# Optimization experiments

Measured on AMD Instinct MI355X. Metric: run time of the kernel, lower is better.

The kernel has to match this reference:

```python
import jax, jax.numpy as jnp
import numpy as np

NUM_ITEMS = 50000
IN_FEATS = 64
H_FEATS = 64
NUM_EDGES = 800000


def setup_inputs() -> dict:
    key = jax.random.key(0)
    ks = jax.random.split(key, 12)
    s_in = 1.0 / np.sqrt(IN_FEATS)
    s_h = 1.0 / np.sqrt(H_FEATS)
    return {
        "embed": jax.random.normal(ks[0], (NUM_ITEMS, IN_FEATS), jnp.float32),
        "W1_self": jax.random.normal(ks[1], (IN_FEATS, H_FEATS), jnp.float32) * s_in,
        "W1_neigh": jax.random.normal(ks[2], (IN_FEATS, H_FEATS), jnp.float32) * s_in,
        "b1": jax.random.normal(ks[3], (H_FEATS,), jnp.float32) * s_in,
        "W2_self": jax.random.normal(ks[4], (H_FEATS, H_FEATS), jnp.float32) * s_h,
        "W2_neigh": jax.random.normal(ks[5], (H_FEATS, H_FEATS), jnp.float32) * s_h,
        "b2": jax.random.normal(ks[6], (H_FEATS,), jnp.float32) * s_h,
        "W_fc": jax.random.normal(ks[7], (H_FEATS, IN_FEATS), jnp.float32) * s_h,
        "b_fc": jax.random.normal(ks[8], (IN_FEATS,), jnp.float32) * s_h,
        "item_ids": jnp.arange(NUM_ITEMS, dtype=jnp.int64),
        "src": jax.random.randint(ks[9], (NUM_EDGES,), 0, NUM_ITEMS, jnp.int64),
        "dst": jax.random.randint(ks[10], (NUM_EDGES,), 0, NUM_ITEMS, jnp.int64),
    }


def _sage_mean(h, src, dst, W_self, W_neigh, b, num_nodes):
    # gather src features along edges, mean-reduce into dst nodes
    agg = jax.ops.segment_sum(h[src], dst, num_segments=num_nodes)  # [N, d]
    deg = jax.ops.segment_sum(jnp.ones_like(dst, dtype=h.dtype), dst,
                              num_segments=num_nodes)
    h_neigh = agg / jnp.clip(deg, 1.0, None)[:, None]  # zero for isolated nodes
    return h @ W_self + h_neigh @ W_neigh + b


def reference(embed, W1_self, W1_neigh, b1, W2_self, W2_neigh, b2,
              W_fc, b_fc, item_ids, src, dst):
    n = embed.shape[0]
    x = embed[item_ids]                                   # embedding lookup [N, in]
    h = _sage_mean(x, src, dst, W1_self, W1_neigh, b1, n)  # SAGEConv 1
    h = jax.nn.relu(h)
    h = _sage_mean(h, src, dst, W2_self, W2_neigh, b2, n)  # SAGEConv 2
    return h @ W_fc + b_fc                                 # final linear
```

## Files before the change

kernel.cpp:

```cpp
#include <hip/hip_runtime.h>

#define NN 50000
#define NE 800000
#define F  64
#define AT 68
#define SCAN_B 49

__device__ __forceinline__ unsigned bf16rne(float f) {
    unsigned u = __float_as_uint(f);
    return (u + 0x7fffu + ((u >> 16) & 1u)) >> 16;
}


__global__ void k_count_pos(const int* __restrict__ dst, int* __restrict__ cnt,
                            int* __restrict__ pos) {
    int e = blockIdx.x * blockDim.x + threadIdx.x;
    if (e < NE) pos[e] = atomicAdd(&cnt[dst[e]], 1);
}


__launch_bounds__(256)
__global__ void k_scan_a(const int* __restrict__ cnt, int* __restrict__ partials) {
    __shared__ int sc[256];
    int t = threadIdx.x;
    int base = blockIdx.x * 1024 + t * 4;
    int s = 0;
#pragma unroll
    for (int k = 0; k < 4; ++k) {
        int idx = base + k;
        s += (idx < NN) ? cnt[idx] : 0;
    }
    sc[t] = s;
    __syncthreads();
    for (int d = 128; d > 0; d >>= 1) {
        if (t < d) sc[t] += sc[t + d];
        __syncthreads();
    }
    if (t == 0) partials[blockIdx.x] = sc[0];
}

__launch_bounds__(64)
__global__ void k_scan_b(const int* __restrict__ partials, int* __restrict__ blockoff,
                         int* __restrict__ offs_last) {
    int t = threadIdx.x;
    int v = (t < SCAN_B) ? partials[t] : 0;
    int orig = v;
    for (int d = 1; d < 64; d <<= 1) {
        int u = __shfl_up(v, d);
        if (t >= d) v += u;
    }
    if (t < SCAN_B) blockoff[t] = v - orig;
    if (t == 63) *offs_last = v;
}

__launch_bounds__(256)
__global__ void k_scan_c(const int* __restrict__ cnt, const int* __restrict__ blockoff,
                         int* __restrict__ offs) {
    __shared__ int sc[256];
    int t = threadIdx.x;
    int base = blockIdx.x * 1024 + t * 4;
    int v[4];
#pragma unroll
    for (int k = 0; k < 4; ++k) {
        int idx = base + k;
        v[k] = (idx < NN) ? cnt[idx] : 0;
    }
    int lsum = v[0] + v[1] + v[2] + v[3];
    sc[t] = lsum;
    __syncthreads();
    for (int d = 1; d < 256; d <<= 1) {
        int u = (t >= d) ? sc[t - d] : 0;
        __syncthreads();
        sc[t] += u;
        __syncthreads();
    }
    int run = blockoff[blockIdx.x] + sc[t] - lsum;
#pragma unroll
    for (int k = 0; k < 4; ++k) {
        int idx = base + k;
        if (idx < NN) { offs[idx] = run; run += v[k]; }
    }
}

__global__ void k_fill(const int* __restrict__ src, const int* __restrict__ dst,
                       const int* __restrict__ offs, const int* __restrict__ pos,
                       int* __restrict__ csr) {
    int e = blockIdx.x * blockDim.x + threadIdx.x;
    if (e < NE) csr[offs[dst[e]] + pos[e]] = src[e];
}


__global__ void k_gather(const float* __restrict__ embed, const int* __restrict__ ids,
                         float* __restrict__ x, uint2* __restrict__ xb) {
    int t = blockIdx.x * blockDim.x + threadIdx.x;
    if (t < NN * 16) {
        int i = t >> 4, c = t & 15;
        float4 v = ((const float4*)embed)[ids[i] * 16 + c];
        ((float4*)x)[t] = v;
        uint2 p;
        p.x = bf16rne(v.x) | (bf16rne(v.y) << 16);
        p.y = bf16rne(v.z) | (bf16rne(v.w) << 16);
        xb[t] = p;
    }
}


__device__ __forceinline__ void add8(float s[8], const uint4 v) {
    s[0] += __uint_as_float(v.x << 16);
    s[1] += __uint_as_float(v.x & 0xffff0000u);
    s[2] += __uint_as_float(v.y << 16);
    s[3] += __uint_as_float(v.y & 0xffff0000u);
    s[4] += __uint_as_float(v.z << 16);
    s[5] += __uint_as_float(v.z & 0xffff0000u);
    s[6] += __uint_as_float(v.w << 16);
    s[7] += __uint_as_float(v.w & 0xffff0000u);
}

__launch_bounds__(256)
__global__ void k_aggb(const uint4* __restrict__ inb, const int* __restrict__ offs,
                       const int* __restrict__ csr, float4* __restrict__ hn4) {
    int g = (blockIdx.x * 256 + threadIdx.x) >> 3;
    int c = threadIdx.x & 7;
    if (g >= NN) return;
    int beg = offs[g], end = offs[g + 1];
    float s[8] = {0.f, 0.f, 0.f, 0.f, 0.f, 0.f, 0.f, 0.f};
    int j = beg;
    for (; j + 8 <= end; j += 8) {
        int i0 = csr[j + 0], i1 = csr[j + 1], i2 = csr[j + 2], i3 = csr[j + 3];
        int i4 = csr[j + 4], i5 = csr[j + 5], i6 = csr[j + 6], i7 = csr[j + 7];
        uint4 v0 = inb[i0 * 8 + c], v1 = inb[i1 * 8 + c];
        uint4 v2 = inb[i2 * 8 + c], v3 = inb[i3 * 8 + c];
        uint4 v4 = inb[i4 * 8 + c], v5 = inb[i5 * 8 + c];
        uint4 v6 = inb[i6 * 8 + c], v7 = inb[i7 * 8 + c];
        add8(s, v0); add8(s, v1); add8(s, v2); add8(s, v3);
        add8(s, v4); add8(s, v5); add8(s, v6); add8(s, v7);
    }
    int rem = end - j;
    if (rem > 0) {
        uint4 t[8];
#pragma unroll
        for (int k = 0; k < 8; ++k) {
            int jj = (k < rem) ? j + k : j;
            t[k] = inb[csr[jj] * 8 + c];
        }
#pragma unroll
        for (int k = 0; k < 8; ++k)
            if (k < rem) add8(s, t[k]);
    }
    int deg = end - beg;
    float inv = (deg > 0) ? 1.f / (float)deg : 0.f;
    float4 o0 = make_float4(s[0] * inv, s[1] * inv, s[2] * inv, s[3] * inv);
    float4 o1 = make_float4(s[4] * inv, s[5] * inv, s[6] * inv, s[7] * inv);
    hn4[g * 16 + c * 2 + 0] = o0;
    hn4[g * 16 + c * 2 + 1] = o1;
}


template <bool RELU, bool EMITB>
__launch_bounds__(256)
__global__ void k_layer2(const float* __restrict__ X, const float* __restrict__ Nh,
                         const float* __restrict__ Ws, const float* __restrict__ Wn,
                         const float* __restrict__ b, float* __restrict__ out,
                         uint2* __restrict__ outb) {
    __shared__ alignas(16) float AsT[F * AT];
    __shared__ alignas(16) float NsT[F * AT];
    __shared__ alignas(16) float WsL[F * F];
    __shared__ alignas(16) float WnL[F * F];

    const int tid = threadIdx.x;
    const int node0 = blockIdx.x * 64;

    for (int idx = tid; idx < F * F / 4; idx += 256) {
        ((float4*)WsL)[idx] = ((const float4*)Ws)[idx];
        ((float4*)WnL)[idx] = ((const float4*)Wn)[idx];
    }
    for (int idx = tid; idx < 64 * 16; idx += 256) {
        int n = idx >> 4, c = idx & 15;
        int node = node0 + n;
        float4 a = make_float4(0.f, 0.f, 0.f, 0.f);
        float4 v = make_float4(0.f, 0.f, 0.f, 0.f);
        if (node < NN) {
            a = ((const float4*)X)[node * 16 + c];
            v = ((const float4*)Nh)[node * 16 + c];
        }
        int f = 4 * c;
        AsT[(f + 0) * AT + n] = a.x; AsT[(f + 1) * AT + n] = a.y;
        AsT[(f + 2) * AT + n] = a.z; AsT[(f + 3) * AT + n] = a.w;
        NsT[(f + 0) * AT + n] = v.x; NsT[(f + 1) * AT + n] = v.y;
        NsT[(f + 2) * AT + n] = v.z; NsT[(f + 3) * AT + n] = v.w;
    }
    __syncthreads();

    const int tx = tid & 15, ty = tid >> 4;
    float acc[4][4];
#pragma unroll
    for (int j = 0; j < 4; ++j) {
        float bv = b[4 * tx + j];
        acc[0][j] = bv; acc[1][j] = bv; acc[2][j] = bv; acc[3][j] = bv;
    }
#pragma unroll 4
    for (int k = 0; k < 64; ++k) {
        float4 a4 = *(const float4*)&AsT[k * AT + 4 * ty];
        float4 n4 = *(const float4*)&NsT[k * AT + 4 * ty];
        float4 w4 = *(const float4*)&WsL[k * 64 + 4 * tx];
        float4 u4 = *(const float4*)&WnL[k * 64 + 4 * tx];
        float a_[4] = {a4.x, a4.y, a4.z, a4.w};
        float n_[4] = {n4.x, n4.y, n4.z, n4.w};
        float w_[4] = {w4.x, w4.y, w4.z, w4.w};
        float u_[4] = {u4.x, u4.y, u4.z, u4.w};
#pragma unroll
        for (int i = 0; i < 4; ++i)
#pragma unroll
            for (int j = 0; j < 4; ++j)
                acc[i][j] += a_[i] * w_[j] + n_[i] * u_[j];
    }

#pragma unroll
    for (int i = 0; i < 4; ++i) {
        int node = node0 + 4 * ty + i;
        if (node < NN) {
            float4 o;
            o.x = acc[i][0]; o.y = acc[i][1]; o.z = acc[i][2]; o.w = acc[i][3];
            if (RELU) {
                o.x = o.x > 0.f ? o.x : 0.f;
                o.y = o.y > 0.f ? o.y : 0.f;
                o.z = o.z > 0.f ? o.z : 0.f;
                o.w = o.w > 0.f ? o.w : 0.f;
            }
            *(float4*)&out[node * 64 + 4 * tx] = o;
            if (EMITB) {
                uint2 p;
                p.x = bf16rne(o.x) | (bf16rne(o.y) << 16);
                p.y = bf16rne(o.z) | (bf16rne(o.w) << 16);
                outb[node * 16 + tx] = p;
            }
        }
    }
}


__launch_bounds__(256)
__global__ void k_final(const float* __restrict__ X, const float* __restrict__ W,
                        const float* __restrict__ b, float* __restrict__ out) {
    __shared__ alignas(16) float AsT[F * AT];
    __shared__ alignas(16) float WL[F * F];

    const int tid = threadIdx.x;
    const int node0 = blockIdx.x * 64;

    for (int idx = tid; idx < F * F / 4; idx += 256)
        ((float4*)WL)[idx] = ((const float4*)W)[idx];
    for (int idx = tid; idx < 64 * 16; idx += 256) {
        int n = idx >> 4, c = idx & 15;
        int node = node0 + n;
        float4 a = make_float4(0.f, 0.f, 0.f, 0.f);
        if (node < NN) a = ((const float4*)X)[node * 16 + c];
        int f = 4 * c;
        AsT[(f + 0) * AT + n] = a.x; AsT[(f + 1) * AT + n] = a.y;
        AsT[(f + 2) * AT + n] = a.z; AsT[(f + 3) * AT + n] = a.w;
    }
    __syncthreads();

    const int tx = tid & 15, ty = tid >> 4;
    float acc[4][4];
#pragma unroll
    for (int j = 0; j < 4; ++j) {
        float bv = b[4 * tx + j];
        acc[0][j] = bv; acc[1][j] = bv; acc[2][j] = bv; acc[3][j] = bv;
    }
#pragma unroll 4
    for (int k = 0; k < 64; ++k) {
        float4 a4 = *(const float4*)&AsT[k * AT + 4 * ty];
        float4 w4 = *(const float4*)&WL[k * 64 + 4 * tx];
        float a_[4] = {a4.x, a4.y, a4.z, a4.w};
        float w_[4] = {w4.x, w4.y, w4.z, w4.w};
#pragma unroll
        for (int i = 0; i < 4; ++i)
#pragma unroll
            for (int j = 0; j < 4; ++j)
                acc[i][j] += a_[i] * w_[j];
    }
#pragma unroll
    for (int i = 0; i < 4; ++i) {
        int node = node0 + 4 * ty + i;
        if (node < NN) {
            float4 o;
            o.x = acc[i][0]; o.y = acc[i][1]; o.z = acc[i][2]; o.w = acc[i][3];
            *(float4*)&out[node * 64 + 4 * tx] = o;
        }
    }
}


extern "C" void kernel_launch(void* const* d_in, const int* in_sizes, int n_in,
                              void* d_out, int out_size, void* d_ws, size_t ws_size,
                              hipStream_t stream) {
    const float* embed = (const float*)d_in[0];
    const float* W1s = (const float*)d_in[1];
    const float* W1n = (const float*)d_in[2];
    const float* b1  = (const float*)d_in[3];
    const float* W2s = (const float*)d_in[4];
    const float* W2n = (const float*)d_in[5];
    const float* b2  = (const float*)d_in[6];
    const float* Wfc = (const float*)d_in[7];
    const float* bfc = (const float*)d_in[8];
    const int* ids = (const int*)d_in[9];
    const int* src = (const int*)d_in[10];
    const int* dst = (const int*)d_in[11];
    float* out = (float*)d_out;

    char* ws = (char*)d_ws;
    size_t off = 0;
    auto alloc = [&](size_t nb) {
        char* p = ws + off;
        off = (off + nb + 255) & ~(size_t)255;
        return p;
    };
    int*   cnt      = (int*)alloc(NN * sizeof(int));
    size_t zero_bytes = off;
    int*   offs     = (int*)alloc((NN + 1) * sizeof(int));
    int*   partials = (int*)alloc(SCAN_B * sizeof(int));
    int*   blockoff = (int*)alloc(SCAN_B * sizeof(int));
    int*   pos      = (int*)alloc(NE * sizeof(int));
    int*   csr      = (int*)alloc(NE * sizeof(int));
    float* x        = (float*)alloc((size_t)NN * F * sizeof(float));
    float* h1       = (float*)alloc((size_t)NN * F * sizeof(float));
    float* hn       = (float*)alloc((size_t)NN * F * sizeof(float));
    uint2* xb       = (uint2*)alloc((size_t)NN * 16 * sizeof(uint2));
    uint2* h1b      = (uint2*)alloc((size_t)NN * 16 * sizeof(uint2));
    float* h2       = x;

    hipMemsetAsync(d_ws, 0, zero_bytes, stream);

    const int TB = 256;
    k_count_pos<<<(NE + TB - 1) / TB, TB, 0, stream>>>(dst, cnt, pos);
    k_scan_a<<<SCAN_B, 256, 0, stream>>>(cnt, partials);
    k_scan_b<<<1, 64, 0, stream>>>(partials, blockoff, &offs[NN]);
    k_scan_c<<<SCAN_B, 256, 0, stream>>>(cnt, blockoff, offs);
    k_fill<<<(NE + TB - 1) / TB, TB, 0, stream>>>(src, dst, offs, pos, csr);
    k_gather<<<(NN * 16 + TB - 1) / TB, TB, 0, stream>>>(embed, ids, x, xb);

    const int NB = (NN + 63) / 64;
    const int AB = (NN * 8 + 255) / 256;

    k_aggb<<<AB, TB, 0, stream>>>((const uint4*)xb, offs, csr, (float4*)hn);
    k_layer2<true, true><<<NB, TB, 0, stream>>>(x, hn, W1s, W1n, b1, h1, h1b);
    k_aggb<<<AB, TB, 0, stream>>>((const uint4*)h1b, offs, csr, (float4*)hn);
    k_layer2<false, false><<<NB, TB, 0, stream>>>(h1, hn, W2s, W2n, b2, h2, nullptr);
    k_final<<<NB, TB, 0, stream>>>(h2, Wfc, bfc, out);
}
```

Measured before the change: 239.1 us.

## Cut memory traffic: bf16 neighbor means, drop fp32 x copy, cursor-based CSR fill

The neighbor-mean output of the aggregation kernel is now stored as bf16 instead of fp32, which halves its write and read traffic, and the layer kernel unpacks it into shared memory. The fp32 copy of the gathered embeddings is removed, so layer 1 reads embed through ids directly. CSR fill now uses an atomic cursor copied from offs rather than a stored per-edge position array, which avoids writing and reading 800K ints. Column indices in the aggregation loop are loaded cooperatively once per group and broadcast with shuffles. The costs are extra rounding of the neighbor means, a second set of atomics in the fill, and a non-deterministic edge order within each row.

```diff
diff --git a/kernel.cpp b/kernel.cpp
--- a/kernel.cpp
+++ b/kernel.cpp
@@ -10,12 +10,13 @@
     unsigned u = __float_as_uint(f);
     return (u + 0x7fffu + ((u >> 16) & 1u)) >> 16;
 }
-
-
-__global__ void k_count_pos(const int* __restrict__ dst, int* __restrict__ cnt,
-                            int* __restrict__ pos) {
+__device__ __forceinline__ float bflo(unsigned p) { return __uint_as_float(p << 16); }
+__device__ __forceinline__ float bfhi(unsigned p) { return __uint_as_float(p & 0xffff0000u); }
+
+
+__global__ void k_count(const int* __restrict__ dst, int* __restrict__ cnt) {
     int e = blockIdx.x * blockDim.x + threadIdx.x;
-    if (e < NE) pos[e] = atomicAdd(&cnt[dst[e]], 1);
+    if (e < NE) atomicAdd(&cnt[dst[e]], 1);
 }
 
 
@@ -83,20 +84,21 @@
 }
 
 __global__ void k_fill(const int* __restrict__ src, const int* __restrict__ dst,
-                       const int* __restrict__ offs, const int* __restrict__ pos,
-                       int* __restrict__ csr) {
+                       int* __restrict__ cursor, int* __restrict__ csr) {
     int e = blockIdx.x * blockDim.x + threadIdx.x;
-    if (e < NE) csr[offs[dst[e]] + pos[e]] = src[e];
+    if (e < NE) {
+        int p = atomicAdd(&cursor[dst[e]], 1);
+        csr[p] = src[e];
+    }
 }
 
 
 __global__ void k_gather(const float* __restrict__ embed, const int* __restrict__ ids,
-                         float* __restrict__ x, uint2* __restrict__ xb) {
+                         uint2* __restrict__ xb) {
     int t = blockIdx.x * blockDim.x + threadIdx.x;
     if (t < NN * 16) {
         int i = t >> 4, c = t & 15;
         float4 v = ((const float4*)embed)[ids[i] * 16 + c];
-        ((float4*)x)[t] = v;
         uint2 p;
         p.x = bf16rne(v.x) | (bf16rne(v.y) << 16);
         p.y = bf16rne(v.z) | (bf16rne(v.w) << 16);
@@ -106,59 +108,61 @@
 
 
 __device__ __forceinline__ void add8(float s[8], const uint4 v) {
-    s[0] += __uint_as_float(v.x << 16);
-    s[1] += __uint_as_float(v.x & 0xffff0000u);
-    s[2] += __uint_as_float(v.y << 16);
-    s[3] += __uint_as_float(v.y & 0xffff0000u);
-    s[4] += __uint_as_float(v.z << 16);
-    s[5] += __uint_as_float(v.z & 0xffff0000u);
-    s[6] += __uint_as_float(v.w << 16);
-    s[7] += __uint_as_float(v.w & 0xffff0000u);
+    s[0] += bflo(v.x); s[1] += bfhi(v.x);
+    s[2] += bflo(v.y); s[3] += bfhi(v.y);
+    s[4] += bflo(v.z); s[5] += bfhi(v.z);
+    s[6] += bflo(v.w); s[7] += bfhi(v.w);
 }
 
 __launch_bounds__(256)
 __global__ void k_aggb(const uint4* __restrict__ inb, const int* __restrict__ offs,
-                       const int* __restrict__ csr, float4* __restrict__ hn4) {
+                       const int* __restrict__ csr, uint4* __restrict__ hnb) {
     int g = (blockIdx.x * 256 + threadIdx.x) >> 3;
     int c = threadIdx.x & 7;
     if (g >= NN) return;
+    int lane = threadIdx.x & 63;
+    int base = lane & 56;
     int beg = offs[g], end = offs[g + 1];
     float s[8] = {0.f, 0.f, 0.f, 0.f, 0.f, 0.f, 0.f, 0.f};
     int j = beg;
     for (; j + 8 <= end; j += 8) {
-        int i0 = csr[j + 0], i1 = csr[j + 1], i2 = csr[j + 2], i3 = csr[j + 3];
-        int i4 = csr[j + 4], i5 = csr[j + 5], i6 = csr[j + 6], i7 = csr[j + 7];
-        uint4 v0 = inb[i0 * 8 + c], v1 = inb[i1 * 8 + c];
-        uint4 v2 = inb[i2 * 8 + c], v3 = inb[i3 * 8 + c];
-        uint4 v4 = inb[i4 * 8 + c], v5 = inb[i5 * 8 + c];
-        uint4 v6 = inb[i6 * 8 + c], v7 = inb[i7 * 8 + c];
-        add8(s, v0); add8(s, v1); add8(s, v2); add8(s, v3);
-        add8(s, v4); add8(s, v5); add8(s, v6); add8(s, v7);
+        int v = csr[j + c];
+        int i0 = __shfl(v, base + 0, 64), i1 = __shfl(v, base + 1, 64);
+        int i2 = __shfl(v, base + 2, 64), i3 = __shfl(v, base + 3, 64);
+        int i4 = __shfl(v, base + 4, 64), i5 = __shfl(v, base + 5, 64);
+        int i6 = __shfl(v, base + 6, 64), i7 = __shfl(v, base + 7, 64);
+        uint4 d0 = inb[i0 * 8 + c], d1 = inb[i1 * 8 + c];
+        uint4 d2 = inb[i2 * 8 + c], d3 = inb[i3 * 8 + c];
+        uint4 d4 = inb[i4 * 8 + c], d5 = inb[i5 * 8 + c];
+        uint4 d6 = inb[i6 * 8 + c], d7 = inb[i7 * 8 + c];
+        add8(s, d0); add8(s, d1); add8(s, d2); add8(s, d3);
+        add8(s, d4); add8(s, d5); add8(s, d6); add8(s, d7);
     }
     int rem = end - j;
     if (rem > 0) {
-        uint4 t[8];
-#pragma unroll
-        for (int k = 0; k < 8; ++k) {
-            int jj = (k < rem) ? j + k : j;
-            t[k] = inb[csr[jj] * 8 + c];
-        }
+        int v = csr[j + (c < rem ? c : 0)];
+        int idx[8];
+#pragma unroll
+        for (int k = 0; k < 8; ++k) idx[k] = __shfl(v, base + k, 64);
 #pragma unroll
         for (int k = 0; k < 8; ++k)
-            if (k < rem) add8(s, t[k]);
+            if (k < rem) { uint4 d = inb[idx[k] * 8 + c]; add8(s, d); }
     }
     int deg = end - beg;
     float inv = (deg > 0) ? 1.f / (float)deg : 0.f;
-    float4 o0 = make_float4(s[0] * inv, s[1] * inv, s[2] * inv, s[3] * inv);
-    float4 o1 = make_float4(s[4] * inv, s[5] * inv, s[6] * inv, s[7] * inv);
-    hn4[g * 16 + c * 2 + 0] = o0;
-    hn4[g * 16 + c * 2 + 1] = o1;
+    uint4 o;
+    o.x = bf16rne(s[0] * inv) | (bf16rne(s[1] * inv) << 16);
+    o.y = bf16rne(s[2] * inv) | (bf16rne(s[3] * inv) << 16);
+    o.z = bf16rne(s[4] * inv) | (bf16rne(s[5] * inv) << 16);
+    o.w = bf16rne(s[6] * inv) | (bf16rne(s[7] * inv) << 16);
+    hnb[g * 8 + c] = o;
 }
 
 
 template <bool RELU, bool EMITB>
 __launch_bounds__(256)
-__global__ void k_layer2(const float* __restrict__ X, const float* __restrict__ Nh,
+__global__ void k_layer2(const float* __restrict__ X, const int* __restrict__ ids,
+                         const uint4* __restrict__ Nhb,
                          const float* __restrict__ Ws, const float* __restrict__ Wn,
                          const float* __restrict__ b, float* __restrict__ out,
                          uint2* __restrict__ outb) {
@@ -178,16 +182,24 @@
         int n = idx >> 4, c = idx & 15;
         int node = node0 + n;
         float4 a = make_float4(0.f, 0.f, 0.f, 0.f);
-        float4 v = make_float4(0.f, 0.f, 0.f, 0.f);
         if (node < NN) {
-            a = ((const float4*)X)[node * 16 + c];
-            v = ((const float4*)Nh)[node * 16 + c];
+            int row = ids ? ids[node] : node;
+            a = ((const float4*)X)[row * 16 + c];
         }
         int f = 4 * c;
         AsT[(f + 0) * AT + n] = a.x; AsT[(f + 1) * AT + n] = a.y;
         AsT[(f + 2) * AT + n] = a.z; AsT[(f + 3) * AT + n] = a.w;
-        NsT[(f + 0) * AT + n] = v.x; NsT[(f + 1) * AT + n] = v.y;
-        NsT[(f + 2) * AT + n] = v.z; NsT[(f + 3) * AT + n] = v.w;
+    }
+    for (int idx = tid; idx < 64 * 8; idx += 256) {
+        int n = idx >> 3, c = idx & 7;
+        int node = node0 + n;
+        uint4 v = make_uint4(0u, 0u, 0u, 0u);
+        if (node < NN) v = Nhb[node * 8 + c];
+        int f = 8 * c;
+        NsT[(f + 0) * AT + n] = bflo(v.x); NsT[(f + 1) * AT + n] = bfhi(v.x);
+        NsT[(f + 2) * AT + n] = bflo(v.y); NsT[(f + 3) * AT + n] = bfhi(v.y);
+        NsT[(f + 4) * AT + n] = bflo(v.z); NsT[(f + 5) * AT + n] = bfhi(v.z);
+        NsT[(f + 6) * AT + n] = bflo(v.w); NsT[(f + 7) * AT + n] = bfhi(v.w);
     }
     __syncthreads();
 
@@ -319,33 +331,33 @@
     int*   cnt      = (int*)alloc(NN * sizeof(int));
     size_t zero_bytes = off;
     int*   offs     = (int*)alloc((NN + 1) * sizeof(int));
+    int*   cursor   = (int*)alloc(NN * sizeof(int));
     int*   partials = (int*)alloc(SCAN_B * sizeof(int));
     int*   blockoff = (int*)alloc(SCAN_B * sizeof(int));
-    int*   pos      = (int*)alloc(NE * sizeof(int));
     int*   csr      = (int*)alloc(NE * sizeof(int));
-    float* x        = (float*)alloc((size_t)NN * F * sizeof(float));
-    float* h1       = (float*)alloc((size_t)NN * F * sizeof(float));
-    float* hn       = (float*)alloc((size_t)NN * F * sizeof(float));
     uint2* xb       = (uint2*)alloc((size_t)NN * 16 * sizeof(uint2));
     uint2* h1b      = (uint2*)alloc((size_t)NN * 16 * sizeof(uint2));
-    float* h2       = x;
+    uint4* hnb      = (uint4*)alloc((size_t)NN * 8 * sizeof(uint4));
+    float* h1       = (float*)alloc((size_t)NN * F * sizeof(float));
+    float* h2       = (float*)alloc((size_t)NN * F * sizeof(float));
 
     hipMemsetAsync(d_ws, 0, zero_bytes, stream);
 
     const int TB = 256;
-    k_count_pos<<<(NE + TB - 1) / TB, TB, 0, stream>>>(dst, cnt, pos);
+    k_count<<<(NE + TB - 1) / TB, TB, 0, stream>>>(dst, cnt);
     k_scan_a<<<SCAN_B, 256, 0, stream>>>(cnt, partials);
     k_scan_b<<<1, 64, 0, stream>>>(partials, blockoff, &offs[NN]);
     k_scan_c<<<SCAN_B, 256, 0, stream>>>(cnt, blockoff, offs);
-    k_fill<<<(NE + TB - 1) / TB, TB, 0, stream>>>(src, dst, offs, pos, csr);
-    k_gather<<<(NN * 16 + TB - 1) / TB, TB, 0, stream>>>(embed, ids, x, xb);
+    hipMemcpyAsync(cursor, offs, NN * sizeof(int), hipMemcpyDeviceToDevice, stream);
+    k_fill<<<(NE + TB - 1) / TB, TB, 0, stream>>>(src, dst, cursor, csr);
+    k_gather<<<(NN * 16 + TB - 1) / TB, TB, 0, stream>>>(embed, ids, xb);
 
     const int NB = (NN + 63) / 64;
     const int AB = (NN * 8 + 255) / 256;
 
-    k_aggb<<<AB, TB, 0, stream>>>((const uint4*)xb, offs, csr, (float4*)hn);
-    k_layer2<true, true><<<NB, TB, 0, stream>>>(x, hn, W1s, W1n, b1, h1, h1b);
-    k_aggb<<<AB, TB, 0, stream>>>((const uint4*)h1b, offs, csr, (float4*)hn);
-    k_layer2<false, false><<<NB, TB, 0, stream>>>(h1, hn, W2s, W2n, b2, h2, nullptr);
+    k_aggb<<<AB, TB, 0, stream>>>((const uint4*)xb, offs, csr, hnb);
+    k_layer2<true, true><<<NB, TB, 0, stream>>>(embed, ids, hnb, W1s, W1n, b1, h1, h1b);
+    k_aggb<<<AB, TB, 0, stream>>>((const uint4*)h1b, offs, csr, hnb);
+    k_layer2<false, false><<<NB, TB, 0, stream>>>(h1, nullptr, hnb, W2s, W2n, b2, h2, nullptr);
     k_final<<<NB, TB, 0, stream>>>(h2, Wfc, bfc, out);
 }
```

Result: slower. 284.0 us (+18.8%).
